# Kernel tuning notes

Measured on AMD Instinct MI355X. Metric: run time of the kernel, lower is better.

Reference implementation:

```python
import jax, jax.numpy as jnp
from jax import lax
import numpy as np

V, H, L, C, T = 32000, 1024, 256, 32, 64
SOS_TOKEN = 0


def _lstm_cell(h, c, x, Wih, Whh, bih, bhh):
    # h,c,x: [1,H]; Wih,Whh: [4H,H] (torch gate order i,f,g,o)
    g = x @ Wih.T + h @ Whh.T + bih + bhh
    i, f, gg, o = jnp.split(g, 4, axis=-1)
    c = jax.nn.sigmoid(f) * c + jax.nn.sigmoid(i) * jnp.tanh(gg)
    h = jax.nn.sigmoid(o) * jnp.tanh(c)
    return h, c


def setup_inputs() -> dict:
    key = jax.random.key(0)
    ks = jax.random.split(key, 24)
    s = 1.0 / np.sqrt(H)
    n = lambda k, shp, sc: (jax.random.normal(k, shp, dtype=jnp.float32) * sc)
    return {
        "word": jax.random.randint(ks[0], (1, T), 0, V),
        "tense": jax.random.randint(ks[1], (1,), 0, 4),
        "use_teacher_forcing": 1,
        "tense_emb": n(ks[2], (4, C), 0.02),
        "enc_emb": n(ks[3], (V, H), 0.02),
        "enc_Wih": n(ks[4], (4 * H, H), s),
        "enc_Whh": n(ks[5], (4 * H, H), s),
        "enc_bih": n(ks[6], (4 * H,), s),
        "enc_bhh": n(ks[7], (4 * H,), s),
        "W_mean": n(ks[8], (L, H), s),
        "b_mean": n(ks[9], (L,), s),
        "W_var": n(ks[10], (L, H), s),
        "b_var": n(ks[11], (L,), s),
        "W_l2h": n(ks[12], (H, L + C), s),
        "b_l2h": n(ks[13], (H,), s),
        "dec_emb": n(ks[14], (V, H), 0.02),
        "dec_Wih": n(ks[15], (4 * H, H), s),
        "dec_Whh": n(ks[16], (4 * H, H), s),
        "dec_bih": n(ks[17], (4 * H,), s),
        "dec_bhh": n(ks[18], (4 * H,), s),
        "W_out": n(ks[19], (V, H), s),
        "b_out": n(ks[20], (V,), s),
        "eps": jax.random.normal(ks[21], (L,), dtype=jnp.float32),
    }


def reference(word, tense, use_teacher_forcing, tense_emb, enc_emb, enc_Wih,
              enc_Whh, enc_bih, enc_bhh, W_mean, b_mean, W_var, b_var,
              W_l2h, b_l2h, dec_emb, dec_Wih, dec_Whh, dec_bih, dec_bhh,
              W_out, b_out, eps):
    tense_e = tense_emb[tense]                       # [1, C]
    # Encoder: initial hidden = [zeros(H-C) | tense_emb]
    h0 = jnp.concatenate([jnp.zeros((1, H - C), tense_e.dtype), tense_e], axis=-1)
    c0 = jnp.zeros((1, H), tense_e.dtype)
    enc_x = enc_emb[word[0]]                         # [T, H]

    def enc_step(carry, x):
        h, c = _lstm_cell(carry[0], carry[1], x[None], enc_Wih, enc_Whh, enc_bih, enc_bhh)
        return (h, c), None

    (h, _c), _ = lax.scan(enc_step, (h0, c0), enc_x)
    mean = h @ W_mean.T + b_mean                     # [1, L]
    logvar = h @ W_var.T + b_var                     # [1, L]
    latent = mean + eps * jnp.exp(0.5 * logvar)      # reparameterize

    dec_h0 = jnp.concatenate([latent, tense_e], axis=-1) @ W_l2h.T + b_l2h  # [1,H]
    dec_c0 = jnp.zeros((1, H), dec_h0.dtype)

    # teacher forcing: inputs are [SOS, word[0][0], ..., word[0][T-2]]
    dec_in = jnp.concatenate([jnp.full((1,), SOS_TOKEN, word.dtype), word[0, :-1]])
    dec_x = jax.nn.relu(dec_emb[dec_in])             # [T, H]

    def dec_step(carry, x):
        h, c = _lstm_cell(carry[0], carry[1], x[None], dec_Wih, dec_Whh, dec_bih, dec_bhh)
        logits = h @ W_out.T + b_out                 # [1, V]
        return (h, c), jax.nn.log_softmax(logits, axis=-1)[0]

    _, pred_distribution = lax.scan(dec_step, (dec_h0, dec_c0), dec_x)  # [T, V]
    pred_output = jnp.argmax(pred_distribution, axis=1)                 # [T]
    return pred_output, pred_distribution, mean, logvar
```

## Files before the change

kernel.cpp:

```cpp
#include <hip/hip_runtime.h>
#include <math.h>

#define Hd 1024
#define Td 64
#define Vd 32000

static const size_t OFF_GENC  = 131072;
static const size_t OFF_GDEC  = 393216;
static const size_t OFF_TEN   = 663552;
static const size_t OFF_HALL  = 663584;
static const size_t OFF_MB    = 730144;
static const size_t OFF_ST2   = 1000000;

#define MB_H_PAIRS  133120u
#define MB_PAIRS    133376u
#define FLAGB       0x3f800000u

__device__ __forceinline__ float fsigm(float x) {
  return __fdividef(1.f, 1.f + __expf(-x));
}
__device__ __forceinline__ float ftanh(float x) {
  return 1.f - __fdividef(2.f, __expf(2.f * x) + 1.f);
}

__device__ __forceinline__ void st_flag(unsigned long long* p, float v) {
  unsigned long long u = 0x3f80000000000000ull | (unsigned long long)__float_as_uint(v);
  __hip_atomic_store(p, u, __ATOMIC_RELAXED, __HIP_MEMORY_SCOPE_AGENT);
}

__device__ __forceinline__ float4 poll16(const float2* p) {
  float4 a;
  for (;;) {
    asm volatile("global_load_dwordx4 %0, %1, off sc0 sc1\n\ts_waitcnt vmcnt(0)"
                 : "=&v"(a) : "v"(p) : "memory");
    if (__float_as_uint(a.y) == FLAGB && __float_as_uint(a.w) == FLAGB) return a;
  }
}

__device__ __forceinline__ void stage1024(const float2* base, float* dst, int tid) {
  float4 a = poll16(base + 2 * tid);
  ((float2*)dst)[tid] = make_float2(a.x, a.z);
  __syncthreads();
}

__device__ __forceinline__ void gemm_gather_body(const float* __restrict__ W,
                                                 const float* __restrict__ emb,
                                                 const int* __restrict__ word, int dec_mode,
                                                 const float* __restrict__ bih,
                                                 const float* __restrict__ bhh,
                                                 float* __restrict__ out, int R, int rbase) {
  __shared__ float xs[64][68];
  __shared__ float wsh[64][68];
  const int tid = threadIdx.x;
  const int a = tid >> 4;
  const int b = tid & 15;
  const int sr = tid & 63;
  const int kq = (tid >> 6) << 4;
  const int tok = dec_mode ? ((sr == 0) ? 0 : word[sr - 1]) : word[sr];
  const float* xrow = emb + (size_t)tok * 1024;
  float acc[4][4];
#pragma unroll
  for (int i = 0; i < 4; ++i)
#pragma unroll
    for (int q = 0; q < 4; ++q) acc[i][q] = 0.f;

  for (int kc = 0; kc < 1024; kc += 64) {
    const float4* gx = (const float4*)(xrow + kc + kq);
    const float4* gw = (const float4*)(W + (size_t)(rbase + sr) * 1024 + kc + kq);
    float4 vx0 = gx[0], vx1 = gx[1], vx2 = gx[2], vx3 = gx[3];
    float4 vw0 = gw[0], vw1 = gw[1], vw2 = gw[2], vw3 = gw[3];
    if (dec_mode) {
      vx0.x = fmaxf(vx0.x, 0.f); vx0.y = fmaxf(vx0.y, 0.f); vx0.z = fmaxf(vx0.z, 0.f); vx0.w = fmaxf(vx0.w, 0.f);
      vx1.x = fmaxf(vx1.x, 0.f); vx1.y = fmaxf(vx1.y, 0.f); vx1.z = fmaxf(vx1.z, 0.f); vx1.w = fmaxf(vx1.w, 0.f);
      vx2.x = fmaxf(vx2.x, 0.f); vx2.y = fmaxf(vx2.y, 0.f); vx2.z = fmaxf(vx2.z, 0.f); vx2.w = fmaxf(vx2.w, 0.f);
      vx3.x = fmaxf(vx3.x, 0.f); vx3.y = fmaxf(vx3.y, 0.f); vx3.z = fmaxf(vx3.z, 0.f); vx3.w = fmaxf(vx3.w, 0.f);
    }
    __syncthreads();
    xs[kq +  0][sr] = vx0.x; xs[kq +  1][sr] = vx0.y; xs[kq +  2][sr] = vx0.z; xs[kq +  3][sr] = vx0.w;
    xs[kq +  4][sr] = vx1.x; xs[kq +  5][sr] = vx1.y; xs[kq +  6][sr] = vx1.z; xs[kq +  7][sr] = vx1.w;
    xs[kq +  8][sr] = vx2.x; xs[kq +  9][sr] = vx2.y; xs[kq + 10][sr] = vx2.z; xs[kq + 11][sr] = vx2.w;
    xs[kq + 12][sr] = vx3.x; xs[kq + 13][sr] = vx3.y; xs[kq + 14][sr] = vx3.z; xs[kq + 15][sr] = vx3.w;
    wsh[kq +  0][sr] = vw0.x; wsh[kq +  1][sr] = vw0.y; wsh[kq +  2][sr] = vw0.z; wsh[kq +  3][sr] = vw0.w;
    wsh[kq +  4][sr] = vw1.x; wsh[kq +  5][sr] = vw1.y; wsh[kq +  6][sr] = vw1.z; wsh[kq +  7][sr] = vw1.w;
    wsh[kq +  8][sr] = vw2.x; wsh[kq +  9][sr] = vw2.y; wsh[kq + 10][sr] = vw2.z; wsh[kq + 11][sr] = vw2.w;
    wsh[kq + 12][sr] = vw3.x; wsh[kq + 13][sr] = vw3.y; wsh[kq + 14][sr] = vw3.z; wsh[kq + 15][sr] = vw3.w;
    __syncthreads();
#pragma unroll 8
    for (int kk = 0; kk < 64; ++kk) {
      float4 xv = *(const float4*)&xs[kk][a * 4];
      float4 wv = *(const float4*)&wsh[kk][b * 4];
      acc[0][0] = fmaf(xv.x, wv.x, acc[0][0]); acc[0][1] = fmaf(xv.x, wv.y, acc[0][1]);
      acc[0][2] = fmaf(xv.x, wv.z, acc[0][2]); acc[0][3] = fmaf(xv.x, wv.w, acc[0][3]);
      acc[1][0] = fmaf(xv.y, wv.x, acc[1][0]); acc[1][1] = fmaf(xv.y, wv.y, acc[1][1]);
      acc[1][2] = fmaf(xv.y, wv.z, acc[1][2]); acc[1][3] = fmaf(xv.y, wv.w, acc[1][3]);
      acc[2][0] = fmaf(xv.z, wv.x, acc[2][0]); acc[2][1] = fmaf(xv.z, wv.y, acc[2][1]);
      acc[2][2] = fmaf(xv.z, wv.z, acc[2][2]); acc[2][3] = fmaf(xv.z, wv.w, acc[2][3]);
      acc[3][0] = fmaf(xv.w, wv.x, acc[3][0]); acc[3][1] = fmaf(xv.w, wv.y, acc[3][1]);
      acc[3][2] = fmaf(xv.w, wv.z, acc[3][2]); acc[3][3] = fmaf(xv.w, wv.w, acc[3][3]);
    }
  }
  const int rb = rbase + b * 4;
  float4 b1 = *(const float4*)(bih + rb);
  float4 b2 = *(const float4*)(bhh + rb);
#pragma unroll
  for (int i = 0; i < 4; ++i) {
    int t = a * 4 + i;
    float4 o;
    o.x = acc[i][0] + b1.x + b2.x; o.y = acc[i][1] + b1.y + b2.y;
    o.z = acc[i][2] + b1.z + b2.z; o.w = acc[i][3] + b1.w + b2.w;
    *(float4*)(out + (size_t)t * R + rb) = o;
  }
}

__global__ __launch_bounds__(256, 2) void gemm_dual_kernel(
    const int* __restrict__ tense, const float* __restrict__ tense_emb,
    const float* __restrict__ enc_emb, const float* __restrict__ dec_emb,
    const int* __restrict__ word,
    const float* __restrict__ W0, const float* __restrict__ bih0,
    const float* __restrict__ bhh0, float* __restrict__ o0,
    const float* __restrict__ W1, const float* __restrict__ bih1,
    const float* __restrict__ bhh1, float* __restrict__ o1,
    float* __restrict__ ws) {
  {
    int gid = blockIdx.x * blockDim.x + threadIdx.x;
    int gsz = gridDim.x * blockDim.x;
    int tens = tense[0];
    if (gid < 32) ws[OFF_TEN + gid] = tense_emb[tens * 32 + gid];
    float2* mb = (float2*)(ws + OFF_MB);
    for (int i = gid; i < (int)MB_PAIRS; i += gsz) {
      float2 v;
      if (i < (int)MB_H_PAIRS && (i >> 10) == 0) {
        int j = i & 1023;
        v.x = (j < Hd - 32) ? 0.f : tense_emb[tens * 32 + (j - (Hd - 32))];
        v.y = 1.0f;
      } else { v.x = 0.f; v.y = 0.f; }
      mb[i] = v;
    }
  }
  if (blockIdx.x < 64)
    gemm_gather_body(W0, enc_emb, word, 0, bih0, bhh0, o0, 4096, blockIdx.x * 64);
  else
    gemm_gather_body(W1, dec_emb, word, 1, bih1, bhh1, o1, 4096, (blockIdx.x - 64) * 64);
}

__global__ __launch_bounds__(256, 2) void gemm_kernel(const float* __restrict__ W,
                                                      const float* __restrict__ x,
                                                      const float* __restrict__ bias,
                                                      float* __restrict__ out, int R,
                                                      float* __restrict__ sd) {
  __shared__ float xs[64][68];
  __shared__ float wsh[64][68];
  const int tid = threadIdx.x;
  const int a = tid >> 4;
  const int b = tid & 15;
  const int sr = tid & 63;
  const int kq = (tid >> 6) << 4;
  const int rbase = blockIdx.x * 64;
  float acc[4][4];
#pragma unroll
  for (int i = 0; i < 4; ++i)
#pragma unroll
    for (int q = 0; q < 4; ++q) acc[i][q] = 0.f;

  for (int kc = 0; kc < 1024; kc += 64) {
    const float4* gx = (const float4*)(x + (size_t)sr * 1024 + kc + kq);
    const float4* gw = (const float4*)(W + (size_t)(rbase + sr) * 1024 + kc + kq);
    float4 vx0 = gx[0], vx1 = gx[1], vx2 = gx[2], vx3 = gx[3];
    float4 vw0 = gw[0], vw1 = gw[1], vw2 = gw[2], vw3 = gw[3];
    __syncthreads();
    xs[kq +  0][sr] = vx0.x; xs[kq +  1][sr] = vx0.y; xs[kq +  2][sr] = vx0.z; xs[kq +  3][sr] = vx0.w;
    xs[kq +  4][sr] = vx1.x; xs[kq +  5][sr] = vx1.y; xs[kq +  6][sr] = vx1.z; xs[kq +  7][sr] = vx1.w;
    xs[kq +  8][sr] = vx2.x; xs[kq +  9][sr] = vx2.y; xs[kq + 10][sr] = vx2.z; xs[kq + 11][sr] = vx2.w;
    xs[kq + 12][sr] = vx3.x; xs[kq + 13][sr] = vx3.y; xs[kq + 14][sr] = vx3.z; xs[kq + 15][sr] = vx3.w;
    wsh[kq +  0][sr] = vw0.x; wsh[kq +  1][sr] = vw0.y; wsh[kq +  2][sr] = vw0.z; wsh[kq +  3][sr] = vw0.w;
    wsh[kq +  4][sr] = vw1.x; wsh[kq +  5][sr] = vw1.y; wsh[kq +  6][sr] = vw1.z; wsh[kq +  7][sr] = vw1.w;
    wsh[kq +  8][sr] = vw2.x; wsh[kq +  9][sr] = vw2.y; wsh[kq + 10][sr] = vw2.z; wsh[kq + 11][sr] = vw2.w;
    wsh[kq + 12][sr] = vw3.x; wsh[kq + 13][sr] = vw3.y; wsh[kq + 14][sr] = vw3.z; wsh[kq + 15][sr] = vw3.w;
    __syncthreads();
#pragma unroll 8
    for (int kk = 0; kk < 64; ++kk) {
      float4 xv = *(const float4*)&xs[kk][a * 4];
      float4 wv = *(const float4*)&wsh[kk][b * 4];
      acc[0][0] = fmaf(xv.x, wv.x, acc[0][0]); acc[0][1] = fmaf(xv.x, wv.y, acc[0][1]);
      acc[0][2] = fmaf(xv.x, wv.z, acc[0][2]); acc[0][3] = fmaf(xv.x, wv.w, acc[0][3]);
      acc[1][0] = fmaf(xv.y, wv.x, acc[1][0]); acc[1][1] = fmaf(xv.y, wv.y, acc[1][1]);
      acc[1][2] = fmaf(xv.y, wv.z, acc[1][2]); acc[1][3] = fmaf(xv.y, wv.w, acc[1][3]);
      acc[2][0] = fmaf(xv.z, wv.x, acc[2][0]); acc[2][1] = fmaf(xv.z, wv.y, acc[2][1]);
      acc[2][2] = fmaf(xv.z, wv.z, acc[2][2]); acc[2][3] = fmaf(xv.z, wv.w, acc[2][3]);
      acc[3][0] = fmaf(xv.w, wv.x, acc[3][0]); acc[3][1] = fmaf(xv.w, wv.y, acc[3][1]);
      acc[3][2] = fmaf(xv.w, wv.z, acc[3][2]); acc[3][3] = fmaf(xv.w, wv.w, acc[3][3]);
    }
  }
  const int rb = rbase + b * 4;
  float4 bv = *(const float4*)(bias + rb);
#pragma unroll
  for (int i = 0; i < 4; ++i) {
    int t = a * 4 + i;
    float4 o;
    o.x = acc[i][0] + bv.x; o.y = acc[i][1] + bv.y;
    o.z = acc[i][2] + bv.z; o.w = acc[i][3] + bv.w;
    *(float4*)(out + (size_t)t * R + rb) = o;
    float m = o.x; int mi = rb;
    if (o.y > m) { m = o.y; mi = rb + 1; }
    if (o.z > m) { m = o.z; mi = rb + 2; }
    if (o.w > m) { m = o.w; mi = rb + 3; }
    float s = __expf(o.x - m) + __expf(o.y - m) + __expf(o.z - m) + __expf(o.w - m);
#pragma unroll
    for (int off = 1; off < 16; off <<= 1) {
      float om = __shfl_xor(m, off, 64);
      int   oi = __shfl_xor(mi, off, 64);
      float os = __shfl_xor(s, off, 64);
      if (om > m || (om == m && oi < mi)) {
        s = os + s * __expf(m - om);
        m = om; mi = oi;
      } else {
        s = s + os * __expf(om - m);
      }
    }
    if (b == 0) {
      float* p = sd + ((size_t)t * 500 + blockIdx.x) * 4;
      p[0] = m; p[1] = (float)mi; p[2] = s;
    }
  }
}

__device__ __forceinline__ void gload16(const float* base, float* d) {
  asm volatile(
      "global_load_dword %0, %16, off\n\t"
      "global_load_dword %1, %16, off offset:256\n\t"
      "global_load_dword %2, %16, off offset:512\n\t"
      "global_load_dword %3, %16, off offset:768\n\t"
      "global_load_dword %4, %16, off offset:1024\n\t"
      "global_load_dword %5, %16, off offset:1280\n\t"
      "global_load_dword %6, %16, off offset:1536\n\t"
      "global_load_dword %7, %16, off offset:1792\n\t"
      "global_load_dword %8, %16, off offset:2048\n\t"
      "global_load_dword %9, %16, off offset:2304\n\t"
      "global_load_dword %10, %16, off offset:2560\n\t"
      "global_load_dword %11, %16, off offset:2816\n\t"
      "global_load_dword %12, %16, off offset:3072\n\t"
      "global_load_dword %13, %16, off offset:3328\n\t"
      "global_load_dword %14, %16, off offset:3584\n\t"
      "global_load_dword %15, %16, off offset:3840\n\t"
      "s_waitcnt vmcnt(0)"
      : "=&v"(d[0]), "=&v"(d[1]), "=&v"(d[2]), "=&v"(d[3]),
        "=&v"(d[4]), "=&v"(d[5]), "=&v"(d[6]), "=&v"(d[7]),
        "=&v"(d[8]), "=&v"(d[9]), "=&v"(d[10]), "=&v"(d[11]),
        "=&v"(d[12]), "=&v"(d[13]), "=&v"(d[14]), "=&v"(d[15])
      : "v"(base));
}

__global__ __launch_bounds__(512, 2) void seq_kernel(
    const float* __restrict__ enc_Whh, const float* __restrict__ dec_Whh,
    const float* __restrict__ W_mean, const float* __restrict__ b_mean,
    const float* __restrict__ W_var, const float* __restrict__ b_var,
    const float* __restrict__ W_l2h, const float* __restrict__ b_l2h,
    const float* __restrict__ eps, float* __restrict__ ws, float* __restrict__ dout) {
  __shared__ float hsbuf[2][Hd];
  __shared__ float lat[288];
  const int tid = threadIdx.x;
  const int lane = tid & 63;
  const int wid = tid >> 6;
  const int j = blockIdx.x * 8 + wid;

  float2* mb = (float2*)(ws + OFF_MB);
  unsigned long long* mbq = (unsigned long long*)(ws + OFF_MB);
  const float* Genc = ws + OFF_GENC;
  const float* Gdec = ws + OFF_GDEC;
  float* h_all = ws + OFF_HALL;

  float we[4][16], wd[4][16];
#pragma unroll
  for (int r = 0; r < 4; ++r) {
    const size_t ro = (size_t)(r * Hd + j) * Hd + lane;
    gload16(enc_Whh + ro, we[r]);
    gload16(dec_Whh + ro, wd[r]);
  }

  float c_reg = 0.f;
  float gb0 = Genc[j], gb1 = Genc[1024 + j], gb2 = Genc[2048 + j], gb3 = Genc[3072 + j];
  for (int t = 0; t < Td; ++t) {
    stage1024(mb + (size_t)t * 1024, hsbuf[t & 1], tid);
    const float* hs = hsbuf[t & 1];
    float p0 = 0.f, p1 = 0.f, p2 = 0.f, p3 = 0.f;
#pragma unroll
    for (int i = 0; i < 16; ++i) {
      float hv = hs[lane + 64 * i];
      p0 = fmaf(we[0][i], hv, p0);
      p1 = fmaf(we[1][i], hv, p1);
      p2 = fmaf(we[2][i], hv, p2);
      p3 = fmaf(we[3][i], hv, p3);
    }
#pragma unroll
    for (int off = 32; off; off >>= 1) {
      p0 += __shfl_xor(p0, off, 64); p1 += __shfl_xor(p1, off, 64);
      p2 += __shfl_xor(p2, off, 64); p3 += __shfl_xor(p3, off, 64);
    }
    float gi = gb0 + p0, gf = gb1 + p1, gg = gb2 + p2, go = gb3 + p3;
    c_reg = fsigm(gf) * c_reg + fsigm(gi) * ftanh(gg);
    float hval = fsigm(go) * ftanh(c_reg);
    if (lane == 0) st_flag(mbq + (size_t)(t + 1) * 1024 + j, hval);
    if (t + 1 < Td) {
      gb0 = Genc[(t + 1) * 4096 + j];
      gb1 = Genc[(t + 1) * 4096 + 1024 + j];
      gb2 = Genc[(t + 1) * 4096 + 2048 + j];
      gb3 = Genc[(t + 1) * 4096 + 3072 + j];
    }
  }

  if (j < 256) {
    stage1024(mb + (size_t)Td * 1024, hsbuf[0], tid);
    const float* hs = hsbuf[0];
    const float* Wm = W_mean + (size_t)j * Hd;
    const float* Wv = W_var + (size_t)j * Hd;
    float pm = 0.f, pv = 0.f;
#pragma unroll
    for (int i = 0; i < 16; ++i) {
      float hv = hs[lane + 64 * i];
      pm = fmaf(Wm[lane + 64 * i], hv, pm);
      pv = fmaf(Wv[lane + 64 * i], hv, pv);
    }
#pragma unroll
    for (int off = 32; off; off >>= 1) {
      pm += __shfl_xor(pm, off, 64); pv += __shfl_xor(pv, off, 64);
    }
    if (lane == 0) {
      float m = pm + b_mean[j];
      float lv = pv + b_var[j];
      dout[2048064 + j] = m;
      dout[2048320 + j] = lv;
      float latv = m + eps[j] * __expf(0.5f * lv);
      st_flag(mbq + MB_H_PAIRS + j, latv);
    }
  }

  if (tid < 128) {
    float4 a = poll16(mb + MB_H_PAIRS + 2 * tid);
    lat[2 * tid] = a.x; lat[2 * tid + 1] = a.z;
  } else if (tid < 160) {
    lat[256 + (tid - 128)] = ws[OFF_TEN + (tid - 128)];
  }
  __syncthreads();

  {
    const float* Wr = W_l2h + (size_t)j * 288;
    float p = fmaf(Wr[lane], lat[lane], 0.f);
    p = fmaf(Wr[lane + 64], lat[lane + 64], p);
    p = fmaf(Wr[lane + 128], lat[lane + 128], p);
    p = fmaf(Wr[lane + 192], lat[lane + 192], p);
    if (lane < 32) p = fmaf(Wr[lane + 256], lat[lane + 256], p);
#pragma unroll
    for (int off = 32; off; off >>= 1) p += __shfl_xor(p, off, 64);
    if (lane == 0) st_flag(mbq + (size_t)65 * 1024 + j, p + b_l2h[j]);
  }
  __syncthreads();

  c_reg = 0.f;
  gb0 = Gdec[j]; gb1 = Gdec[1024 + j]; gb2 = Gdec[2048 + j]; gb3 = Gdec[3072 + j];
  for (int t = 0; t < Td; ++t) {
    stage1024(mb + (size_t)(65 + t) * 1024, hsbuf[t & 1], tid);
    const float* hs = hsbuf[t & 1];
    float p0 = 0.f, p1 = 0.f, p2 = 0.f, p3 = 0.f;
#pragma unroll
    for (int i = 0; i < 16; ++i) {
      float hv = hs[lane + 64 * i];
      p0 = fmaf(wd[0][i], hv, p0);
      p1 = fmaf(wd[1][i], hv, p1);
      p2 = fmaf(wd[2][i], hv, p2);
      p3 = fmaf(wd[3][i], hv, p3);
    }
#pragma unroll
    for (int off = 32; off; off >>= 1) {
      p0 += __shfl_xor(p0, off, 64); p1 += __shfl_xor(p1, off, 64);
      p2 += __shfl_xor(p2, off, 64); p3 += __shfl_xor(p3, off, 64);
    }
    float gi = gb0 + p0, gf = gb1 + p1, gg = gb2 + p2, go = gb3 + p3;
    c_reg = fsigm(gf) * c_reg + fsigm(gi) * ftanh(gg);
    float hval = fsigm(go) * ftanh(c_reg);
    if (lane == 0) {
      if (t + 1 < Td) st_flag(mbq + (size_t)(66 + t) * 1024 + j, hval);
      h_all[(size_t)t * Hd + j] = hval;
    }
    if (t + 1 < Td) {
      gb0 = Gdec[(t + 1) * 4096 + j];
      gb1 = Gdec[(t + 1) * 4096 + 1024 + j];
      gb2 = Gdec[(t + 1) * 4096 + 2048 + j];
      gb3 = Gdec[(t + 1) * 4096 + 3072 + j];
    }
  }
}

__global__ __launch_bounds__(256) void lfin_kernel(float* __restrict__ out,
                                                   const float* __restrict__ sd) {
  const int blk = blockIdx.x, t = blk >> 2, q = blk & 3, tid = threadIdx.x;
  __shared__ float sm[256];
  __shared__ float ss[256];
  __shared__ int si[256];
  float M = -INFINITY, S = 0.f; int MI = 0x7fffffff;
  for (int k = tid; k < 500; k += 256) {
    const float* p = sd + ((size_t)t * 500 + k) * 4;
    float m = p[0]; int mi = (int)p[1]; float s = p[2];
    if (m > M || (m == M && mi < MI)) {
      S = s + S * __expf(M - m);
      M = m; MI = mi;
    } else {
      S = S + s * __expf(m - M);
    }
  }
  sm[tid] = M; si[tid] = MI; ss[tid] = S;
  __syncthreads();
  for (int st = 128; st > 0; st >>= 1) {
    if (tid < st) {
      float om = sm[tid + st]; int oi = si[tid + st]; float os = ss[tid + st];
      if (om > sm[tid] || (om == sm[tid] && oi < si[tid])) {
        ss[tid] = os + ss[tid] * __expf(sm[tid] - om);
        sm[tid] = om; si[tid] = oi;
      } else {
        ss[tid] = ss[tid] + os * __expf(om - sm[tid]);
      }
    }
    __syncthreads();
  }
  float corr = sm[0] + logf(ss[0]);
  float4* r4 = (float4*)(out + 64 + (size_t)t * Vd + q * 8000);
  for (int i = tid; i < 2000; i += 256) {
    float4 v = r4[i];
    v.x -= corr; v.y -= corr; v.z -= corr; v.w -= corr;
    r4[i] = v;
  }
  if (q == 0 && tid == 0) out[t] = (float)si[0];
}

extern "C" void kernel_launch(void* const* d_in, const int* in_sizes, int n_in,
                              void* d_out, int out_size, void* d_ws, size_t ws_size,
                              hipStream_t stream) {
  (void)in_sizes; (void)n_in; (void)out_size; (void)ws_size;
  const int* word       = (const int*)d_in[0];
  const int* tense      = (const int*)d_in[1];
  const float* tense_emb = (const float*)d_in[3];
  const float* enc_emb   = (const float*)d_in[4];
  const float* enc_Wih   = (const float*)d_in[5];
  const float* enc_Whh   = (const float*)d_in[6];
  const float* enc_bih   = (const float*)d_in[7];
  const float* enc_bhh   = (const float*)d_in[8];
  const float* W_mean    = (const float*)d_in[9];
  const float* b_mean    = (const float*)d_in[10];
  const float* W_var     = (const float*)d_in[11];
  const float* b_var     = (const float*)d_in[12];
  const float* W_l2h     = (const float*)d_in[13];
  const float* b_l2h     = (const float*)d_in[14];
  const float* dec_emb   = (const float*)d_in[15];
  const float* dec_Wih   = (const float*)d_in[16];
  const float* dec_Whh   = (const float*)d_in[17];
  const float* dec_bih   = (const float*)d_in[18];
  const float* dec_bhh   = (const float*)d_in[19];
  const float* W_out     = (const float*)d_in[20];
  const float* b_out     = (const float*)d_in[21];
  const float* eps       = (const float*)d_in[22];
  float* out = (float*)d_out;
  float* ws  = (float*)d_ws;

  gemm_dual_kernel<<<128, 256, 0, stream>>>(tense, tense_emb, enc_emb, dec_emb, word,
                                            enc_Wih, enc_bih, enc_bhh, ws + OFF_GENC,
                                            dec_Wih, dec_bih, dec_bhh, ws + OFF_GDEC, ws);
  seq_kernel<<<128, 512, 0, stream>>>(enc_Whh, dec_Whh, W_mean, b_mean, W_var, b_var,
                                      W_l2h, b_l2h, eps, ws, out);
  gemm_kernel<<<500, 256, 0, stream>>>(W_out, ws + OFF_HALL, b_out, out + 64, 32000,
                                       ws + OFF_ST2);
  lfin_kernel<<<256, 256, 0, stream>>>(out, ws + OFF_ST2);
}
```

Before: 508.6 us.

## Split input-projection GEMM over K halves and use DPP wave reductions

The input-projection GEMM for encoder and decoder is split into two K-halves, doubling the grid from 128 to 256 blocks, with each half writing its own partial buffer (bih folded into one half, bhh into the other). The sequential LSTM kernel then sums both partials per gate. The shuffle-based 64-lane reductions in the recurrent steps are replaced with a DPP-based reduction that leaves the result in lane 63, which now publishes h. This trades extra partial-buffer reads per step for more GEMM parallelism and cheaper cross-lane reductions on the serial critical path.

```diff
diff --git a/kernel.cpp b/kernel.cpp
--- a/kernel.cpp
+++ b/kernel.cpp
@@ -5,12 +5,14 @@
 #define Td 64
 #define Vd 32000
 
-static const size_t OFF_GENC  = 131072;
-static const size_t OFF_GDEC  = 393216;
-static const size_t OFF_TEN   = 663552;
-static const size_t OFF_HALL  = 663584;
-static const size_t OFF_MB    = 730144;
-static const size_t OFF_ST2   = 1000000;
+static const size_t OFF_GENC0 = 0;
+static const size_t OFF_GENC1 = 262144;
+static const size_t OFF_GDEC0 = 524288;
+static const size_t OFF_GDEC1 = 786432;
+static const size_t OFF_TEN   = 1048576;
+static const size_t OFF_HALL  = 1048640;
+static const size_t OFF_MB    = 1114176;
+static const size_t OFF_ST2   = 1380928;
 
 #define MB_H_PAIRS  133120u
 #define MB_PAIRS    133376u
@@ -43,12 +45,21 @@
   __syncthreads();
 }
 
+__device__ __forceinline__ float dpp_sum64(float x) {
+  x += __int_as_float(__builtin_amdgcn_update_dpp(0, __float_as_int(x), 0xB1,  0xf, 0xf, true));
+  x += __int_as_float(__builtin_amdgcn_update_dpp(0, __float_as_int(x), 0x4E,  0xf, 0xf, true));
+  x += __int_as_float(__builtin_amdgcn_update_dpp(0, __float_as_int(x), 0x114, 0xf, 0xf, true));
+  x += __int_as_float(__builtin_amdgcn_update_dpp(0, __float_as_int(x), 0x118, 0xf, 0xf, true));
+  x += __int_as_float(__builtin_amdgcn_update_dpp(0, __float_as_int(x), 0x142, 0xa, 0xf, true));
+  x += __int_as_float(__builtin_amdgcn_update_dpp(0, __float_as_int(x), 0x143, 0xc, 0xf, true));
+  return x;
+}
+
 __device__ __forceinline__ void gemm_gather_body(const float* __restrict__ W,
                                                  const float* __restrict__ emb,
                                                  const int* __restrict__ word, int dec_mode,
-                                                 const float* __restrict__ bih,
-                                                 const float* __restrict__ bhh,
-                                                 float* __restrict__ out, int R, int rbase) {
+                                                 const float* __restrict__ bias,
+                                                 float* __restrict__ out, int rbase, int kbase) {
   __shared__ float xs[64][68];
   __shared__ float wsh[64][68];
   const int tid = threadIdx.x;
@@ -64,7 +75,7 @@
 #pragma unroll
     for (int q = 0; q < 4; ++q) acc[i][q] = 0.f;
 
-  for (int kc = 0; kc < 1024; kc += 64) {
+  for (int kc = kbase; kc < kbase + 512; kc += 64) {
     const float4* gx = (const float4*)(xrow + kc + kq);
     const float4* gw = (const float4*)(W + (size_t)(rbase + sr) * 1024 + kc + kq);
     float4 vx0 = gx[0], vx1 = gx[1], vx2 = gx[2], vx3 = gx[3];
@@ -100,15 +111,14 @@
     }
   }
   const int rb = rbase + b * 4;
-  float4 b1 = *(const float4*)(bih + rb);
-  float4 b2 = *(const float4*)(bhh + rb);
+  float4 bv = *(const float4*)(bias + rb);
 #pragma unroll
   for (int i = 0; i < 4; ++i) {
     int t = a * 4 + i;
     float4 o;
-    o.x = acc[i][0] + b1.x + b2.x; o.y = acc[i][1] + b1.y + b2.y;
-    o.z = acc[i][2] + b1.z + b2.z; o.w = acc[i][3] + b1.w + b2.w;
-    *(float4*)(out + (size_t)t * R + rb) = o;
+    o.x = acc[i][0] + bv.x; o.y = acc[i][1] + bv.y;
+    o.z = acc[i][2] + bv.z; o.w = acc[i][3] + bv.w;
+    *(float4*)(out + (size_t)t * 4096 + rb) = o;
   }
 }
 
@@ -116,10 +126,10 @@
     const int* __restrict__ tense, const float* __restrict__ tense_emb,
     const float* __restrict__ enc_emb, const float* __restrict__ dec_emb,
     const int* __restrict__ word,
-    const float* __restrict__ W0, const float* __restrict__ bih0,
-    const float* __restrict__ bhh0, float* __restrict__ o0,
-    const float* __restrict__ W1, const float* __restrict__ bih1,
-    const float* __restrict__ bhh1, float* __restrict__ o1,
+    const float* __restrict__ enc_Wih, const float* __restrict__ enc_bih,
+    const float* __restrict__ enc_bhh,
+    const float* __restrict__ dec_Wih, const float* __restrict__ dec_bih,
+    const float* __restrict__ dec_bhh,
     float* __restrict__ ws) {
   {
     int gid = blockIdx.x * blockDim.x + threadIdx.x;
@@ -137,10 +147,16 @@
       mb[i] = v;
     }
   }
-  if (blockIdx.x < 64)
-    gemm_gather_body(W0, enc_emb, word, 0, bih0, bhh0, o0, 4096, blockIdx.x * 64);
+  const int quad = blockIdx.x >> 6;
+  const int rbase = (blockIdx.x & 63) * 64;
+  if (quad == 0)
+    gemm_gather_body(enc_Wih, enc_emb, word, 0, enc_bih, ws + OFF_GENC0, rbase, 0);
+  else if (quad == 1)
+    gemm_gather_body(enc_Wih, enc_emb, word, 0, enc_bhh, ws + OFF_GENC1, rbase, 512);
+  else if (quad == 2)
+    gemm_gather_body(dec_Wih, dec_emb, word, 1, dec_bih, ws + OFF_GDEC0, rbase, 0);
   else
-    gemm_gather_body(W1, dec_emb, word, 1, bih1, bhh1, o1, 4096, (blockIdx.x - 64) * 64);
+    gemm_gather_body(dec_Wih, dec_emb, word, 1, dec_bhh, ws + OFF_GDEC1, rbase, 512);
 }
 
 __global__ __launch_bounds__(256, 2) void gemm_kernel(const float* __restrict__ W,
@@ -265,8 +281,10 @@
 
   float2* mb = (float2*)(ws + OFF_MB);
   unsigned long long* mbq = (unsigned long long*)(ws + OFF_MB);
-  const float* Genc = ws + OFF_GENC;
-  const float* Gdec = ws + OFF_GDEC;
+  const float* Ge0 = ws + OFF_GENC0;
+  const float* Ge1 = ws + OFF_GENC1;
+  const float* Gd0 = ws + OFF_GDEC0;
+  const float* Gd1 = ws + OFF_GDEC1;
   float* h_all = ws + OFF_HALL;
 
   float we[4][16], wd[4][16];
@@ -278,7 +296,8 @@
   }
 
   float c_reg = 0.f;
-  float gb0 = Genc[j], gb1 = Genc[1024 + j], gb2 = Genc[2048 + j], gb3 = Genc[3072 + j];
+  float ga0 = Ge0[j], ga1 = Ge0[1024 + j], ga2 = Ge0[2048 + j], ga3 = Ge0[3072 + j];
+  float gb0 = Ge1[j], gb1 = Ge1[1024 + j], gb2 = Ge1[2048 + j], gb3 = Ge1[3072 + j];
   for (int t = 0; t < Td; ++t) {
     stage1024(mb + (size_t)t * 1024, hsbuf[t & 1], tid);
     const float* hs = hsbuf[t & 1];
@@ -291,20 +310,18 @@
       p2 = fmaf(we[2][i], hv, p2);
       p3 = fmaf(we[3][i], hv, p3);
     }
-#pragma unroll
-    for (int off = 32; off; off >>= 1) {
-      p0 += __shfl_xor(p0, off, 64); p1 += __shfl_xor(p1, off, 64);
-      p2 += __shfl_xor(p2, off, 64); p3 += __shfl_xor(p3, off, 64);
-    }
-    float gi = gb0 + p0, gf = gb1 + p1, gg = gb2 + p2, go = gb3 + p3;
+    p0 = dpp_sum64(p0); p1 = dpp_sum64(p1);
+    p2 = dpp_sum64(p2); p3 = dpp_sum64(p3);
+    float gi = ga0 + gb0 + p0, gf = ga1 + gb1 + p1;
+    float gg = ga2 + gb2 + p2, go = ga3 + gb3 + p3;
     c_reg = fsigm(gf) * c_reg + fsigm(gi) * ftanh(gg);
     float hval = fsigm(go) * ftanh(c_reg);
-    if (lane == 0) st_flag(mbq + (size_t)(t + 1) * 1024 + j, hval);
+    if (lane == 63) st_flag(mbq + (size_t)(t + 1) * 1024 + j, hval);
     if (t + 1 < Td) {
-      gb0 = Genc[(t + 1) * 4096 + j];
-      gb1 = Genc[(t + 1) * 4096 + 1024 + j];
-      gb2 = Genc[(t + 1) * 4096 + 2048 + j];
-      gb3 = Genc[(t + 1) * 4096 + 3072 + j];
+      ga0 = Ge0[(t + 1) * 4096 + j]; ga1 = Ge0[(t + 1) * 4096 + 1024 + j];
+      ga2 = Ge0[(t + 1) * 4096 + 2048 + j]; ga3 = Ge0[(t + 1) * 4096 + 3072 + j];
+      gb0 = Ge1[(t + 1) * 4096 + j]; gb1 = Ge1[(t + 1) * 4096 + 1024 + j];
+      gb2 = Ge1[(t + 1) * 4096 + 2048 + j]; gb3 = Ge1[(t + 1) * 4096 + 3072 + j];
     }
   }
 
@@ -356,7 +373,8 @@
   __syncthreads();
 
   c_reg = 0.f;
-  gb0 = Gdec[j]; gb1 = Gdec[1024 + j]; gb2 = Gdec[2048 + j]; gb3 = Gdec[3072 + j];
+  ga0 = Gd0[j]; ga1 = Gd0[1024 + j]; ga2 = Gd0[2048 + j]; ga3 = Gd0[3072 + j];
+  gb0 = Gd1[j]; gb1 = Gd1[1024 + j]; gb2 = Gd1[2048 + j]; gb3 = Gd1[3072 + j];
   for (int t = 0; t < Td; ++t) {
     stage1024(mb + (size_t)(65 + t) * 1024, hsbuf[t & 1], tid);
     const float* hs = hsbuf[t & 1];
@@ -369,23 +387,21 @@
       p2 = fmaf(wd[2][i], hv, p2);
       p3 = fmaf(wd[3][i], hv, p3);
     }
-#pragma unroll
-    for (int off = 32; off; off >>= 1) {
-      p0 += __shfl_xor(p0, off, 64); p1 += __shfl_xor(p1, off, 64);
-      p2 += __shfl_xor(p2, off, 64); p3 += __shfl_xor(p3, off, 64);
-    }
-    float gi = gb0 + p0, gf = gb1 + p1, gg = gb2 + p2, go = gb3 + p3;
+    p0 = dpp_sum64(p0); p1 = dpp_sum64(p1);
+    p2 = dpp_sum64(p2); p3 = dpp_sum64(p3);
+    float gi = ga0 + gb0 + p0, gf = ga1 + gb1 + p1;
+    float gg = ga2 + gb2 + p2, go = ga3 + gb3 + p3;
     c_reg = fsigm(gf) * c_reg + fsigm(gi) * ftanh(gg);
     float hval = fsigm(go) * ftanh(c_reg);
-    if (lane == 0) {
+    if (lane == 63) {
       if (t + 1 < Td) st_flag(mbq + (size_t)(66 + t) * 1024 + j, hval);
       h_all[(size_t)t * Hd + j] = hval;
     }
     if (t + 1 < Td) {
-      gb0 = Gdec[(t + 1) * 4096 + j];
-      gb1 = Gdec[(t + 1) * 4096 + 1024 + j];
-      gb2 = Gdec[(t + 1) * 4096 + 2048 + j];
-      gb3 = Gdec[(t + 1) * 4096 + 3072 + j];
+      ga0 = Gd0[(t + 1) * 4096 + j]; ga1 = Gd0[(t + 1) * 4096 + 1024 + j];
+      ga2 = Gd0[(t + 1) * 4096 + 2048 + j]; ga3 = Gd0[(t + 1) * 4096 + 3072 + j];
+      gb0 = Gd1[(t + 1) * 4096 + j]; gb1 = Gd1[(t + 1) * 4096 + 1024 + j];
+      gb2 = Gd1[(t + 1) * 4096 + 2048 + j]; gb3 = Gd1[(t + 1) * 4096 + 3072 + j];
     }
   }
 }
@@ -460,9 +476,9 @@
   float* out = (float*)d_out;
   float* ws  = (float*)d_ws;
 
-  gemm_dual_kernel<<<128, 256, 0, stream>>>(tense, tense_emb, enc_emb, dec_emb, word,
-                                            enc_Wih, enc_bih, enc_bhh, ws + OFF_GENC,
-                                            dec_Wih, dec_bih, dec_bhh, ws + OFF_GDEC, ws);
+  gemm_dual_kernel<<<256, 256, 0, stream>>>(tense, tense_emb, enc_emb, dec_emb, word,
+                                            enc_Wih, enc_bih, enc_bhh,
+                                            dec_Wih, dec_bih, dec_bhh, ws);
   seq_kernel<<<128, 512, 0, stream>>>(enc_Whh, dec_Whh, W_mean, b_mean, W_var, b_var,
                                       W_l2h, b_l2h, eps, ws, out);
   gemm_kernel<<<500, 256, 0, stream>>>(W_out, ws + OFF_HALL, b_out, out + 64, 32000,
```

Result: faster. 474.1 us (median of 2 runs) (-6.8%).
